# Kernel tuning notes

Hardware: AMD Instinct MI355X
Metric: run time of the kernel (lower is better)

The kernel has to match this reference:

```python
import jax, jax.numpy as jnp
import numpy as np

N_NODES = 100000
N_EDGES = 3200000
F_IN, F_HID, F_OUT = 128, 64, 2


def setup_inputs() -> dict:
    key = jax.random.key(0)
    k1, k2, k3, k4 = jax.random.split(key, 4)
    x = jax.random.normal(k1, (N_NODES, F_IN), dtype=jnp.float32)
    edge_index = jax.random.randint(k2, (2, N_EDGES), 0, N_NODES, dtype=jnp.int64)
    W1 = jax.random.normal(k3, (F_IN, F_HID), dtype=jnp.float32) * (1.0 / np.sqrt(F_IN))
    b1 = jnp.zeros((F_HID,), dtype=jnp.float32)
    W2 = jax.random.normal(k4, (F_HID, F_OUT), dtype=jnp.float32) * (1.0 / np.sqrt(F_HID))
    b2 = jnp.zeros((F_OUT,), dtype=jnp.float32)
    return {"x": x, "edge_index": edge_index, "W1": W1, "b1": b1, "W2": W2, "b2": b2}


def _gcn_conv(h, W, b, src, dst, norm, n_nodes):
    # linear transform first (PyG GCNConv does x @ W then propagate)
    h = h @ W                                  # [N, F_out]
    msg = h[src] * norm[:, None]               # gather + per-edge scale, [E+N, F_out]
    agg = jax.ops.segment_sum(msg, dst, num_segments=n_nodes)  # scatter-add
    return agg + b


def reference(x, edge_index, W1, b1, W2, b2):
    n = x.shape[0]
    # add self-loops (GCNConv default add_self_loops=True)
    loops = jnp.arange(n, dtype=edge_index.dtype)
    src = jnp.concatenate([edge_index[0], loops])
    dst = jnp.concatenate([edge_index[1], loops])
    # symmetric degree normalization: deg computed on dst after self-loops
    deg = jax.ops.segment_sum(jnp.ones_like(dst, dtype=x.dtype), dst, num_segments=n)
    dinv = jnp.where(deg > 0, jax.lax.rsqrt(deg), 0.0)
    norm = dinv[src] * dinv[dst]               # [E+N]

    h = _gcn_conv(x, W1, b1, src, dst, norm, n)
    h = jax.nn.relu(h)
    # dropout is identity in eval mode (training=False)
    out = _gcn_conv(h, W2, b2, src, dst, norm, n)  # [N, 2]

    # generator_mask = x[:, 0] == 1; keep static shape by masking + flattening
    mask = (x[:, 0] == 1.0).astype(out.dtype)
    return (out * mask[:, None]).reshape(-1)
```

## Files before the change

kernel.cpp:

```cpp
#include <hip/hip_runtime.h>
#include <hip/hip_bf16.h>
#include <math.h>


constexpr int N   = 100000;
constexpr int E   = 3200000;
constexpr int FIN = 128;
constexpr int FH  = 64;

constexpr int NPB = 256;
constexpr int NB  = (N + NPB - 1) / NPB;
constexpr int K   = 6400;
constexpr int NC  = E / K;
constexpr int NXCD = 8;

typedef __attribute__((ext_vector_type(8))) short short8;
typedef __attribute__((ext_vector_type(4))) float f32x4;
typedef __attribute__((ext_vector_type(2))) float f32x2;

__device__ inline short f2bf(float f) {
  unsigned u = __float_as_uint(f);
  return (short)((u + 0x7FFFu + ((u >> 16) & 1u)) >> 16);
}

__device__ inline unsigned char f2fp8(float f) {
  return (unsigned char)(__builtin_amdgcn_cvt_pk_fp8_f32(f, f, 0, false) & 0xFF);
}

__device__ inline int chunk_of(int bid) {
  const int q = NC / NXCD, r = NC % NXCD;
  int xcd = bid & 7, idx = bid >> 3;
  return (xcd < r) ? xcd * (q + 1) + idx : r * (q + 1) + (xcd - r) * q + idx;
}

__global__ __launch_bounds__(512) void k_cnt(const int* __restrict__ dstA,
                                             int* __restrict__ segCnt) {
  __shared__ int bc[NB];
  const int w = chunk_of(blockIdx.x);
  const int base = w * K;
  for (int i = threadIdx.x; i < NB; i += 512) bc[i] = 0;
  __syncthreads();
  for (int i = threadIdx.x; i < K; i += 512)
    atomicAdd(&bc[dstA[base + i] >> 8], 1);
  __syncthreads();
  for (int b = threadIdx.x; b < NB; b += 512) segCnt[b * NC + w] = bc[b];
}

__global__ __launch_bounds__(512) void k_chunkScan(const int* __restrict__ segCnt,
                                                   int* __restrict__ lp,
                                                   int* __restrict__ binTot) {
  __shared__ int sh[512];
  const int b = blockIdx.x;
  const int t = threadIdx.x;
  int v = (t < NC) ? segCnt[b * NC + t] : 0;
  sh[t] = v;
  __syncthreads();
  for (int off = 1; off < 512; off <<= 1) {
    int tv = (t >= off) ? sh[t - off] : 0;
    __syncthreads();
    sh[t] += tv;
    __syncthreads();
  }
  if (t < NC) lp[b * NC + t] = sh[t] - v;
  if (t == 511) binTot[b] = sh[511];
}

__global__ void k_binScan(const int* __restrict__ binTot,
                          int* __restrict__ binBase, int* __restrict__ rowptr) {
  if (threadIdx.x == 0 && blockIdx.x == 0) {
    int s = 0;
    for (int b = 0; b < NB; ++b) { binBase[b] = s; s += binTot[b]; }
    binBase[NB] = s;
    rowptr[N] = s;
  }
}

__global__ __launch_bounds__(1024) void k_scat(const int* __restrict__ srcA,
                                               const int* __restrict__ dstA,
                                               const int* __restrict__ lp,
                                               const int* __restrict__ binBase,
                                               unsigned* __restrict__ binned) {
  __shared__ int lpw[NB];
  __shared__ int cur[NB];
  const int w = chunk_of(blockIdx.x);
  const int base = w * K;
  for (int b = threadIdx.x; b < NB; b += 1024) {
    lpw[b] = binBase[b] + lp[b * NC + w];
    cur[b] = 0;
  }
  __syncthreads();
  for (int i = threadIdx.x; i < K; i += 1024) {
    int s = srcA[base + i];
    int d = dstA[base + i];
    int b = d >> 8;
    int slot = lpw[b] + atomicAdd(&cur[b], 1);
    binned[slot] = ((unsigned)(d & 255) << 17) | (unsigned)s;
  }
}

__global__ __launch_bounds__(1024) void k_fill4(const unsigned* __restrict__ binned,
                                                const int* __restrict__ binBase,
                                                int* __restrict__ rowptr,
                                                float* __restrict__ dinv,
                                                int* __restrict__ csr_src) {
  __shared__ int cnt_s[NPB];
  __shared__ int sh[NPB];
  __shared__ int cur[NPB];
  const int b = blockIdx.x;
  const int t = threadIdx.x;
  const int w0 = binBase[b], w1 = binBase[b + 1];
  if (t < NPB) cnt_s[t] = 0;
  __syncthreads();
  unsigned e0_,e1_,e2_,e3_,e4_,e5_,e6_,e7_,e8_;
  unsigned* ebuf[9] = {&e0_,&e1_,&e2_,&e3_,&e4_,&e5_,&e6_,&e7_,&e8_};
#pragma unroll
  for (int r = 0; r < 9; ++r) {
    int i = w0 + t + r * 1024;
    unsigned e = (i < w1) ? binned[i] : 0xFFFFFFFFu;
    *ebuf[r] = e;
    if (e != 0xFFFFFFFFu) atomicAdd(&cnt_s[e >> 17], 1);
  }
  for (int i = w0 + t + 9 * 1024; i < w1; i += 1024)
    atomicAdd(&cnt_s[binned[i] >> 17], 1);
  __syncthreads();
  int v = 0;
  if (t < NPB) { v = cnt_s[t]; sh[t] = v; }
  __syncthreads();
  for (int off = 1; off < NPB; off <<= 1) {
    int tv = (t < NPB && t >= off) ? sh[t - off] : 0;
    __syncthreads();
    if (t < NPB) sh[t] += tv;
    __syncthreads();
  }
  if (t < NPB) {
    int node = b * NPB + t;
    int start = w0 + sh[t] - v;
    if (node < N) {
      rowptr[node] = start;
      dinv[node] = 1.0f / sqrtf((float)(v + 1));
    }
    cur[t] = start;
  }
  __syncthreads();
#pragma unroll
  for (int r = 0; r < 9; ++r) {
    unsigned e = *ebuf[r];
    if (e != 0xFFFFFFFFu) {
      int p = atomicAdd(&cur[e >> 17], 1);
      csr_src[p] = (int)(e & 0x1FFFFu);
    }
  }
  for (int i = w0 + t + 9 * 1024; i < w1; i += 1024) {
    unsigned e = binned[i];
    int p = atomicAdd(&cur[e >> 17], 1);
    csr_src[p] = (int)(e & 0x1FFFFu);
  }
}

__global__ __launch_bounds__(256) void k_gemm1(const float* __restrict__ x,
                                               const float* __restrict__ W1,
                                               const float* __restrict__ dinv,
                                               unsigned char* __restrict__ m1) {
  __shared__ short8 W1f[16 * 64];
  const int t = threadIdx.x;
  for (int i = t; i < 16 * 64; i += 256) {
    int frag = i >> 6, l = i & 63;
    int s = frag >> 2, j = frag & 3;
    int kb = 32 * s + 8 * (l >> 4);
    int f  = 16 * j + (l & 15);
    short8 v;
#pragma unroll
    for (int e = 0; e < 8; ++e) v[e] = f2bf(W1[(kb + e) * FH + f]);
    W1f[i] = v;
  }
  __syncthreads();
  const int lane = t & 63;
  const int r16 = lane & 15;
  const int g4  = lane >> 4;
  const int nWaves = gridDim.x * 4;
  const int wid = blockIdx.x * 4 + (t >> 6);
  for (int T = wid; T < N / 16; T += nWaves) {
    const float* xrow = x + (size_t)(16 * T + r16) * FIN + 8 * g4;
    f32x4 acc0 = {0,0,0,0}, acc1 = {0,0,0,0}, acc2 = {0,0,0,0}, acc3 = {0,0,0,0};
#pragma unroll
    for (int s = 0; s < 4; ++s) {
      float4 fa = *(const float4*)(xrow + 32 * s);
      float4 fb = *(const float4*)(xrow + 32 * s + 4);
      short8 a;
      a[0] = f2bf(fa.x); a[1] = f2bf(fa.y); a[2] = f2bf(fa.z); a[3] = f2bf(fa.w);
      a[4] = f2bf(fb.x); a[5] = f2bf(fb.y); a[6] = f2bf(fb.z); a[7] = f2bf(fb.w);
      acc0 = __builtin_amdgcn_mfma_f32_16x16x32_bf16(a, W1f[(s*4+0)*64 + lane], acc0, 0, 0, 0);
      acc1 = __builtin_amdgcn_mfma_f32_16x16x32_bf16(a, W1f[(s*4+1)*64 + lane], acc1, 0, 0, 0);
      acc2 = __builtin_amdgcn_mfma_f32_16x16x32_bf16(a, W1f[(s*4+2)*64 + lane], acc2, 0, 0, 0);
      acc3 = __builtin_amdgcn_mfma_f32_16x16x32_bf16(a, W1f[(s*4+3)*64 + lane], acc3, 0, 0, 0);
    }
    const int nodeBase = 16 * T + 4 * g4;
    float dv0 = dinv[nodeBase + 0];
    float dv1 = dinv[nodeBase + 1];
    float dv2 = dinv[nodeBase + 2];
    float dv3 = dinv[nodeBase + 3];
#pragma unroll
    for (int j = 0; j < 4; ++j) {
      f32x4 acc = (j == 0) ? acc0 : (j == 1) ? acc1 : (j == 2) ? acc2 : acc3;
      size_t fcol = 16 * j + r16;
      m1[(size_t)(nodeBase + 0) * FH + fcol] = f2fp8(acc[0] * dv0);
      m1[(size_t)(nodeBase + 1) * FH + fcol] = f2fp8(acc[1] * dv1);
      m1[(size_t)(nodeBase + 2) * FH + fcol] = f2fp8(acc[2] * dv2);
      m1[(size_t)(nodeBase + 3) * FH + fcol] = f2fp8(acc[3] * dv3);
    }
  }
}

__global__ __launch_bounds__(256) void k_agg1(const unsigned char* __restrict__ m1,
                                              const int* __restrict__ rowptr,
                                              const int* __restrict__ csr_src,
                                              const float* __restrict__ dinv,
                                              const float* __restrict__ b1,
                                              const float* __restrict__ W2,
                                              float* __restrict__ m2) {
  const int lane = threadIdx.x & 63;
  const int half = lane >> 5;
  const int nb   = blockIdx.x * 16 + (threadIdx.x >> 6) * 4;
  const int node0 = nb + half;
  const int node1 = nb + 2 + half;
  const int g2 = (lane >> 3) & 3;
  const int q  = lane & 7;
  const int i  = lane & 31;
  const int s00 = rowptr[node0];
  const int deg0 = rowptr[node0 + 1] - s00;
  const int s01 = rowptr[node1];
  const int deg1 = rowptr[node1 + 1] - s01;
  const uint2* __restrict__ m1q = (const uint2*)m1;
  float x0=0,x1=0,x2=0,x3=0,x4=0,x5=0,x6=0,x7=0;
  float y0=0,y1=0,y2=0,y3=0,y4=0,y5=0,y6=0,y7=0;
  for (int base = 0;; base += 32) {
    int rem0 = deg0 - base, rem1 = deg1 - base;
    if (__all((rem0 <= 0) && (rem1 <= 0))) break;
    int sv0 = (i < rem0) ? csr_src[s00 + base + i] : 0;
    int sv1 = (i < rem1) ? csr_src[s01 + base + i] : 0;
#pragma unroll
    for (int j = 0; j < 32; j += 8) {
      int idx = j + g2;
      int sa = __shfl(sv0, (half << 5) | idx);
      int sb = __shfl(sv1, (half << 5) | idx);
      bool pa = idx < rem0, pb = idx < rem1;
      uint2 va, vb;
      if (pa) va = m1q[(size_t)sa * 8 + q];
      if (pb) vb = m1q[(size_t)sb * 8 + q];
      if (pa) {
        f32x2 f0 = __builtin_amdgcn_cvt_pk_f32_fp8(va.x, false);
        f32x2 f1 = __builtin_amdgcn_cvt_pk_f32_fp8(va.x, true);
        f32x2 f2 = __builtin_amdgcn_cvt_pk_f32_fp8(va.y, false);
        f32x2 f3 = __builtin_amdgcn_cvt_pk_f32_fp8(va.y, true);
        x0 += f0.x; x1 += f0.y; x2 += f1.x; x3 += f1.y;
        x4 += f2.x; x5 += f2.y; x6 += f3.x; x7 += f3.y;
      }
      if (pb) {
        f32x2 f0 = __builtin_amdgcn_cvt_pk_f32_fp8(vb.x, false);
        f32x2 f1 = __builtin_amdgcn_cvt_pk_f32_fp8(vb.x, true);
        f32x2 f2 = __builtin_amdgcn_cvt_pk_f32_fp8(vb.y, false);
        f32x2 f3 = __builtin_amdgcn_cvt_pk_f32_fp8(vb.y, true);
        y0 += f0.x; y1 += f0.y; y2 += f1.x; y3 += f1.y;
        y4 += f2.x; y5 += f2.y; y6 += f3.x; y7 += f3.y;
      }
    }
  }
#pragma unroll
  for (int off = 8; off <= 16; off <<= 1) {
    x0 += __shfl_xor(x0, off); x1 += __shfl_xor(x1, off);
    x2 += __shfl_xor(x2, off); x3 += __shfl_xor(x3, off);
    x4 += __shfl_xor(x4, off); x5 += __shfl_xor(x5, off);
    x6 += __shfl_xor(x6, off); x7 += __shfl_xor(x7, off);
    y0 += __shfl_xor(y0, off); y1 += __shfl_xor(y1, off);
    y2 += __shfl_xor(y2, off); y3 += __shfl_xor(y3, off);
    y4 += __shfl_xor(y4, off); y5 += __shfl_xor(y5, off);
    y6 += __shfl_xor(y6, off); y7 += __shfl_xor(y7, off);
  }
  {
    uint2 va = m1q[(size_t)node0 * 8 + q];
    uint2 vb = m1q[(size_t)node1 * 8 + q];
    f32x2 f0 = __builtin_amdgcn_cvt_pk_f32_fp8(va.x, false);
    f32x2 f1 = __builtin_amdgcn_cvt_pk_f32_fp8(va.x, true);
    f32x2 f2 = __builtin_amdgcn_cvt_pk_f32_fp8(va.y, false);
    f32x2 f3 = __builtin_amdgcn_cvt_pk_f32_fp8(va.y, true);
    x0 += f0.x; x1 += f0.y; x2 += f1.x; x3 += f1.y;
    x4 += f2.x; x5 += f2.y; x6 += f3.x; x7 += f3.y;
    f0 = __builtin_amdgcn_cvt_pk_f32_fp8(vb.x, false);
    f1 = __builtin_amdgcn_cvt_pk_f32_fp8(vb.x, true);
    f2 = __builtin_amdgcn_cvt_pk_f32_fp8(vb.y, false);
    f3 = __builtin_amdgcn_cvt_pk_f32_fp8(vb.y, true);
    y0 += f0.x; y1 += f0.y; y2 += f1.x; y3 += f1.y;
    y4 += f2.x; y5 += f2.y; y6 += f3.x; y7 += f3.y;
  }
  const float4 bva = ((const float4*)b1)[q * 2 + 0];
  const float4 bvb = ((const float4*)b1)[q * 2 + 1];
  const float4 wA = ((const float4*)W2)[q * 4 + 0];
  const float4 wB = ((const float4*)W2)[q * 4 + 1];
  const float4 wC = ((const float4*)W2)[q * 4 + 2];
  const float4 wD = ((const float4*)W2)[q * 4 + 3];
  const float dv0 = dinv[node0];
  const float dv1 = dinv[node1];
  float h0 = fmaxf(fmaf(x0, dv0, bva.x), 0.f);
  float h1 = fmaxf(fmaf(x1, dv0, bva.y), 0.f);
  float h2 = fmaxf(fmaf(x2, dv0, bva.z), 0.f);
  float h3 = fmaxf(fmaf(x3, dv0, bva.w), 0.f);
  float h4 = fmaxf(fmaf(x4, dv0, bvb.x), 0.f);
  float h5 = fmaxf(fmaf(x5, dv0, bvb.y), 0.f);
  float h6 = fmaxf(fmaf(x6, dv0, bvb.z), 0.f);
  float h7 = fmaxf(fmaf(x7, dv0, bvb.w), 0.f);
  float p00 = h0 * wA.x + h1 * wA.z + h2 * wB.x + h3 * wB.z
            + h4 * wC.x + h5 * wC.z + h6 * wD.x + h7 * wD.z;
  float p01 = h0 * wA.y + h1 * wA.w + h2 * wB.y + h3 * wB.w
            + h4 * wC.y + h5 * wC.w + h6 * wD.y + h7 * wD.w;
  h0 = fmaxf(fmaf(y0, dv1, bva.x), 0.f);
  h1 = fmaxf(fmaf(y1, dv1, bva.y), 0.f);
  h2 = fmaxf(fmaf(y2, dv1, bva.z), 0.f);
  h3 = fmaxf(fmaf(y3, dv1, bva.w), 0.f);
  h4 = fmaxf(fmaf(y4, dv1, bvb.x), 0.f);
  h5 = fmaxf(fmaf(y5, dv1, bvb.y), 0.f);
  h6 = fmaxf(fmaf(y6, dv1, bvb.z), 0.f);
  h7 = fmaxf(fmaf(y7, dv1, bvb.w), 0.f);
  float p10 = h0 * wA.x + h1 * wA.z + h2 * wB.x + h3 * wB.z
            + h4 * wC.x + h5 * wC.z + h6 * wD.x + h7 * wD.z;
  float p11 = h0 * wA.y + h1 * wA.w + h2 * wB.y + h3 * wB.w
            + h4 * wC.y + h5 * wC.w + h6 * wD.y + h7 * wD.w;
#pragma unroll
  for (int off = 4; off; off >>= 1) {
    p00 += __shfl_xor(p00, off); p01 += __shfl_xor(p01, off);
    p10 += __shfl_xor(p10, off); p11 += __shfl_xor(p11, off);
  }
  if ((lane & 31) == 0) {
    m2[node0 * 2 + 0] = p00 * dv0;
    m2[node0 * 2 + 1] = p01 * dv0;
    m2[node1 * 2 + 0] = p10 * dv1;
    m2[node1 * 2 + 1] = p11 * dv1;
  }
}

__global__ __launch_bounds__(256) void k_agg2(const float* __restrict__ m2,
                                              const int* __restrict__ rowptr,
                                              const int* __restrict__ csr_src,
                                              const float* __restrict__ dinv,
                                              const float* __restrict__ b2,
                                              const float* __restrict__ x,
                                              float* __restrict__ out) {
  const int lane = threadIdx.x & 63;
  const int half = lane >> 5;
  const int node = blockIdx.x * 8 + (threadIdx.x >> 6) * 2 + half;
  const int s0 = rowptr[node];
  const int e0 = rowptr[node + 1];
  float a0 = 0.f, a1 = 0.f;
  for (int e = s0 + (lane & 31); e < e0; e += 32) {
    int s = csr_src[e];
    a0 += m2[s * 2 + 0];
    a1 += m2[s * 2 + 1];
  }
#pragma unroll
  for (int off = 16; off; off >>= 1) {
    a0 += __shfl_xor(a0, off);
    a1 += __shfl_xor(a1, off);
  }
  if ((lane & 31) == 0) {
    a0 += m2[node * 2 + 0];
    a1 += m2[node * 2 + 1];
    float dv = dinv[node];
    float o0 = a0 * dv + b2[0];
    float o1 = a1 * dv + b2[1];
    float msk = (x[(size_t)node * FIN] == 1.0f) ? 1.0f : 0.0f;
    out[node * 2 + 0] = o0 * msk;
    out[node * 2 + 1] = o1 * msk;
  }
}

extern "C" void kernel_launch(void* const* d_in, const int* in_sizes, int n_in,
                              void* d_out, int out_size, void* d_ws, size_t ws_size,
                              hipStream_t stream) {
  const float* x   = (const float*)d_in[0];
  const int*   ei  = (const int*)d_in[1];
  const float* W1  = (const float*)d_in[2];
  const float* b1  = (const float*)d_in[3];
  const float* W2  = (const float*)d_in[4];
  const float* b2  = (const float*)d_in[5];
  float*       out = (float*)d_out;

  char* w = (char*)d_ws;
  auto alloc = [&](size_t bytes) -> char* {
    char* p = w;
    w += (bytes + 255) & ~(size_t)255;
    return p;
  };
  int*            rowptr  = (int*)alloc((size_t)(N + 1) * 4);
  float*          dinv    = (float*)alloc((size_t)N * 4);
  unsigned*       binned  = (unsigned*)alloc((size_t)E * 4);
  int*            segCnt  = (int*)alloc((size_t)NB * NC * 4);
  int*            lp      = (int*)alloc((size_t)NB * NC * 4);
  int*            binTot  = (int*)alloc((size_t)NB * 4);
  int*            binBase = (int*)alloc((size_t)(NB + 1) * 4);
  int*            csr_src = (int*)alloc((size_t)E * 4);
  unsigned char*  m1      = (unsigned char*)alloc((size_t)N * FH);
  float*          m2      = (float*)alloc((size_t)N * 2 * 4);

  const int* srcA = ei;
  const int* dstA = ei + E;

  k_cnt<<<dim3(NC), dim3(512), 0, stream>>>(dstA, segCnt);
  k_chunkScan<<<dim3(NB), dim3(512), 0, stream>>>(segCnt, lp, binTot);
  k_binScan<<<dim3(1), dim3(64), 0, stream>>>(binTot, binBase, rowptr);
  k_scat<<<dim3(NC), dim3(1024), 0, stream>>>(srcA, dstA, lp, binBase, binned);
  k_fill4<<<dim3(NB), dim3(1024), 0, stream>>>(binned, binBase, rowptr, dinv, csr_src);
  k_gemm1<<<dim3(800), dim3(256), 0, stream>>>(x, W1, dinv, m1);
  k_agg1<<<dim3(N / 16), dim3(256), 0, stream>>>(m1, rowptr, csr_src, dinv, b1, W2, m2);
  k_agg2<<<dim3(N / 8), dim3(256), 0, stream>>>(m2, rowptr, csr_src, dinv, b2, x, out);
}
```

Measured before the change: 128.4 us.

## Overlap layer-1 GEMM with degree counting and apply dinv scale in fill

Merges the x@W1 GEMM into the edge-count kernel as extra blocks so it runs concurrently with counting instead of after CSR construction. Because dinv is not yet known, the GEMM writes unscaled fp8 values, and k_fill4 later rereads each row of m1, rescales it by dinv and writes it back. This removes a separate kernel launch and a serial dependency. In exchange it adds an extra m1 read and write pass and double fp8 rounding.

```diff
diff --git a/kernel.cpp b/kernel.cpp
--- a/kernel.cpp
+++ b/kernel.cpp
@@ -13,6 +13,7 @@
 constexpr int K   = 6400;
 constexpr int NC  = E / K;
 constexpr int NXCD = 8;
+constexpr int NGB = 782;
 
 typedef __attribute__((ext_vector_type(8))) short short8;
 typedef __attribute__((ext_vector_type(4))) float f32x4;
@@ -33,17 +34,67 @@
   return (xcd < r) ? xcd * (q + 1) + idx : r * (q + 1) + (xcd - r) * q + idx;
 }
 
-__global__ __launch_bounds__(512) void k_cnt(const int* __restrict__ dstA,
-                                             int* __restrict__ segCnt) {
+__global__ __launch_bounds__(512) void k_cntgemm(const int* __restrict__ dstA,
+                                                 int* __restrict__ segCnt,
+                                                 const float* __restrict__ x,
+                                                 const float* __restrict__ W1,
+                                                 unsigned char* __restrict__ m1) {
   __shared__ int bc[NB];
-  const int w = chunk_of(blockIdx.x);
-  const int base = w * K;
-  for (int i = threadIdx.x; i < NB; i += 512) bc[i] = 0;
-  __syncthreads();
-  for (int i = threadIdx.x; i < K; i += 512)
-    atomicAdd(&bc[dstA[base + i] >> 8], 1);
-  __syncthreads();
-  for (int b = threadIdx.x; b < NB; b += 512) segCnt[b * NC + w] = bc[b];
+  __shared__ short8 W1f[16 * 64];
+  const int t = threadIdx.x;
+  if (blockIdx.x < NC) {
+    const int w = chunk_of(blockIdx.x);
+    const int base = w * K;
+    for (int i = t; i < NB; i += 512) bc[i] = 0;
+    __syncthreads();
+    for (int i = t; i < K; i += 512)
+      atomicAdd(&bc[dstA[base + i] >> 8], 1);
+    __syncthreads();
+    for (int b = t; b < NB; b += 512) segCnt[b * NC + w] = bc[b];
+  } else {
+    for (int i = t; i < 16 * 64; i += 512) {
+      int frag = i >> 6, l = i & 63;
+      int s = frag >> 2, j = frag & 3;
+      int kb = 32 * s + 8 * (l >> 4);
+      int f  = 16 * j + (l & 15);
+      short8 v;
+#pragma unroll
+      for (int e = 0; e < 8; ++e) v[e] = f2bf(W1[(kb + e) * FH + f]);
+      W1f[i] = v;
+    }
+    __syncthreads();
+    const int lane = t & 63;
+    const int r16 = lane & 15;
+    const int g4  = lane >> 4;
+    const int nWaves = NGB * 8;
+    const int wid = (blockIdx.x - NC) * 8 + (t >> 6);
+    for (int T = wid; T < N / 16; T += nWaves) {
+      const float* xrow = x + (size_t)(16 * T + r16) * FIN + 8 * g4;
+      f32x4 acc0 = {0,0,0,0}, acc1 = {0,0,0,0}, acc2 = {0,0,0,0}, acc3 = {0,0,0,0};
+#pragma unroll
+      for (int s = 0; s < 4; ++s) {
+        float4 fa = *(const float4*)(xrow + 32 * s);
+        float4 fb = *(const float4*)(xrow + 32 * s + 4);
+        short8 a;
+        a[0] = f2bf(fa.x); a[1] = f2bf(fa.y); a[2] = f2bf(fa.z); a[3] = f2bf(fa.w);
+        a[4] = f2bf(fb.x); a[5] = f2bf(fb.y); a[6] = f2bf(fb.z); a[7] = f2bf(fb.w);
+        acc0 = __builtin_amdgcn_mfma_f32_16x16x32_bf16(a, W1f[(s*4+0)*64 + lane], acc0, 0, 0, 0);
+        acc1 = __builtin_amdgcn_mfma_f32_16x16x32_bf16(a, W1f[(s*4+1)*64 + lane], acc1, 0, 0, 0);
+        acc2 = __builtin_amdgcn_mfma_f32_16x16x32_bf16(a, W1f[(s*4+2)*64 + lane], acc2, 0, 0, 0);
+        acc3 = __builtin_amdgcn_mfma_f32_16x16x32_bf16(a, W1f[(s*4+3)*64 + lane], acc3, 0, 0, 0);
+      }
+      const int nodeBase = 16 * T + 4 * g4;
+#pragma unroll
+      for (int j = 0; j < 4; ++j) {
+        f32x4 acc = (j == 0) ? acc0 : (j == 1) ? acc1 : (j == 2) ? acc2 : acc3;
+        size_t fcol = 16 * j + r16;
+        m1[(size_t)(nodeBase + 0) * FH + fcol] = f2fp8(acc[0]);
+        m1[(size_t)(nodeBase + 1) * FH + fcol] = f2fp8(acc[1]);
+        m1[(size_t)(nodeBase + 2) * FH + fcol] = f2fp8(acc[2]);
+        m1[(size_t)(nodeBase + 3) * FH + fcol] = f2fp8(acc[3]);
+      }
+    }
+  }
 }
 
 __global__ __launch_bounds__(512) void k_chunkScan(const int* __restrict__ segCnt,
@@ -102,10 +153,12 @@
                                                 const int* __restrict__ binBase,
                                                 int* __restrict__ rowptr,
                                                 float* __restrict__ dinv,
-                                                int* __restrict__ csr_src) {
+                                                int* __restrict__ csr_src,
+                                                unsigned char* __restrict__ m1) {
   __shared__ int cnt_s[NPB];
   __shared__ int sh[NPB];
   __shared__ int cur[NPB];
+  __shared__ float dv_s[NPB];
   const int b = blockIdx.x;
   const int t = threadIdx.x;
   const int w0 = binBase[b], w1 = binBase[b + 1];
@@ -135,11 +188,13 @@
   if (t < NPB) {
     int node = b * NPB + t;
     int start = w0 + sh[t] - v;
+    float dv = 1.0f / sqrtf((float)(v + 1));
     if (node < N) {
       rowptr[node] = start;
-      dinv[node] = 1.0f / sqrtf((float)(v + 1));
+      dinv[node] = dv;
     }
     cur[t] = start;
+    dv_s[t] = dv;
   }
   __syncthreads();
 #pragma unroll
@@ -155,58 +210,24 @@
     int p = atomicAdd(&cur[e >> 17], 1);
     csr_src[p] = (int)(e & 0x1FFFFu);
   }
-}
-
-__global__ __launch_bounds__(256) void k_gemm1(const float* __restrict__ x,
-                                               const float* __restrict__ W1,
-                                               const float* __restrict__ dinv,
-                                               unsigned char* __restrict__ m1) {
-  __shared__ short8 W1f[16 * 64];
-  const int t = threadIdx.x;
-  for (int i = t; i < 16 * 64; i += 256) {
-    int frag = i >> 6, l = i & 63;
-    int s = frag >> 2, j = frag & 3;
-    int kb = 32 * s + 8 * (l >> 4);
-    int f  = 16 * j + (l & 15);
-    short8 v;
-#pragma unroll
-    for (int e = 0; e < 8; ++e) v[e] = f2bf(W1[(kb + e) * FH + f]);
-    W1f[i] = v;
-  }
-  __syncthreads();
-  const int lane = t & 63;
-  const int r16 = lane & 15;
-  const int g4  = lane >> 4;
-  const int nWaves = gridDim.x * 4;
-  const int wid = blockIdx.x * 4 + (t >> 6);
-  for (int T = wid; T < N / 16; T += nWaves) {
-    const float* xrow = x + (size_t)(16 * T + r16) * FIN + 8 * g4;
-    f32x4 acc0 = {0,0,0,0}, acc1 = {0,0,0,0}, acc2 = {0,0,0,0}, acc3 = {0,0,0,0};
-#pragma unroll
-    for (int s = 0; s < 4; ++s) {
-      float4 fa = *(const float4*)(xrow + 32 * s);
-      float4 fb = *(const float4*)(xrow + 32 * s + 4);
-      short8 a;
-      a[0] = f2bf(fa.x); a[1] = f2bf(fa.y); a[2] = f2bf(fa.z); a[3] = f2bf(fa.w);
-      a[4] = f2bf(fb.x); a[5] = f2bf(fb.y); a[6] = f2bf(fb.z); a[7] = f2bf(fb.w);
-      acc0 = __builtin_amdgcn_mfma_f32_16x16x32_bf16(a, W1f[(s*4+0)*64 + lane], acc0, 0, 0, 0);
-      acc1 = __builtin_amdgcn_mfma_f32_16x16x32_bf16(a, W1f[(s*4+1)*64 + lane], acc1, 0, 0, 0);
-      acc2 = __builtin_amdgcn_mfma_f32_16x16x32_bf16(a, W1f[(s*4+2)*64 + lane], acc2, 0, 0, 0);
-      acc3 = __builtin_amdgcn_mfma_f32_16x16x32_bf16(a, W1f[(s*4+3)*64 + lane], acc3, 0, 0, 0);
-    }
-    const int nodeBase = 16 * T + 4 * g4;
-    float dv0 = dinv[nodeBase + 0];
-    float dv1 = dinv[nodeBase + 1];
-    float dv2 = dinv[nodeBase + 2];
-    float dv3 = dinv[nodeBase + 3];
-#pragma unroll
-    for (int j = 0; j < 4; ++j) {
-      f32x4 acc = (j == 0) ? acc0 : (j == 1) ? acc1 : (j == 2) ? acc2 : acc3;
-      size_t fcol = 16 * j + r16;
-      m1[(size_t)(nodeBase + 0) * FH + fcol] = f2fp8(acc[0] * dv0);
-      m1[(size_t)(nodeBase + 1) * FH + fcol] = f2fp8(acc[1] * dv1);
-      m1[(size_t)(nodeBase + 2) * FH + fcol] = f2fp8(acc[2] * dv2);
-      m1[(size_t)(nodeBase + 3) * FH + fcol] = f2fp8(acc[3] * dv3);
+  {
+    int nl = t >> 2;
+    int q4 = t & 3;
+    int node = b * NPB + nl;
+    if (node < N) {
+      float dv = dv_s[nl];
+      uint4* rowp = (uint4*)(m1 + (size_t)node * FH);
+      uint4 vv = rowp[q4];
+      unsigned dw[4] = {vv.x, vv.y, vv.z, vv.w};
+#pragma unroll
+      for (int d = 0; d < 4; ++d) {
+        f32x2 lo = __builtin_amdgcn_cvt_pk_f32_fp8(dw[d], false);
+        f32x2 hi = __builtin_amdgcn_cvt_pk_f32_fp8(dw[d], true);
+        unsigned r0 = __builtin_amdgcn_cvt_pk_fp8_f32(lo.x * dv, lo.y * dv, 0, false);
+        dw[d] = __builtin_amdgcn_cvt_pk_fp8_f32(hi.x * dv, hi.y * dv, r0, true);
+      }
+      vv.x = dw[0]; vv.y = dw[1]; vv.z = dw[2]; vv.w = dw[3];
+      rowp[q4] = vv;
     }
   }
 }
@@ -403,12 +424,12 @@
   const int* srcA = ei;
   const int* dstA = ei + E;
 
-  k_cnt<<<dim3(NC), dim3(512), 0, stream>>>(dstA, segCnt);
+  k_cntgemm<<<dim3(NC + NGB), dim3(512), 0, stream>>>(dstA, segCnt, x, W1, m1);
   k_chunkScan<<<dim3(NB), dim3(512), 0, stream>>>(segCnt, lp, binTot);
   k_binScan<<<dim3(1), dim3(64), 0, stream>>>(binTot, binBase, rowptr);
   k_scat<<<dim3(NC), dim3(1024), 0, stream>>>(srcA, dstA, lp, binBase, binned);
-  k_fill4<<<dim3(NB), dim3(1024), 0, stream>>>(binned, binBase, rowptr, dinv, csr_src);
-  k_gemm1<<<dim3(800), dim3(256), 0, stream>>>(x, W1, dinv, m1);
+  k_fill4<<<dim3(NB), dim3(1024), 0, stream>>>(binned, binBase, rowptr, dinv,
+                                               csr_src, m1);
   k_agg1<<<dim3(N / 16), dim3(256), 0, stream>>>(m1, rowptr, csr_src, dinv, b1, W2, m2);
   k_agg2<<<dim3(N / 8), dim3(256), 0, stream>>>(m2, rowptr, csr_src, dinv, b2, x, out);
 }
```

After: 125.9 us. About the same (-1.9%).
